# Performance work log

Measured on AMD Instinct MI355X. Metric: run time of the kernel, lower is better.

Reference implementation:

```python
import jax, jax.numpy as jnp
import numpy as np

B, S, D = 4, 4096, 64


def setup_inputs() -> dict:
    key = jax.random.key(0)
    ks = jax.random.split(key, 12)
    sc = 1.0 / np.sqrt(D)
    return {
        "q": jax.random.normal(ks[0], (B, S, D), jnp.float32),
        "k": jax.random.normal(ks[1], (B, S, D), jnp.float32),
        "v": jax.random.normal(ks[2], (B, S, D), jnp.float32),
        "attn_mask": jnp.ones((1, 1, 1), jnp.float32),
        "Wq": jax.random.normal(ks[3], (D, D), jnp.float32) * sc,
        "bq": jax.random.normal(ks[4], (D,), jnp.float32) * 0.01,
        "Wk": jax.random.normal(ks[5], (D, D), jnp.float32) * sc,
        "bk": jax.random.normal(ks[6], (D,), jnp.float32) * 0.01,
        "Wv": jax.random.normal(ks[7], (D, D), jnp.float32) * sc,
        "bv": jax.random.normal(ks[8], (D,), jnp.float32) * 0.01,
        "qw": jax.random.normal(ks[9], (1, 1, D), jnp.float32),
        "kw": jax.random.normal(ks[10], (1, 1, D), jnp.float32),
    }


def reference(q, k, v, attn_mask, Wq, bq, Wk, bk, Wv, bv, qw, kw):
    d = q.shape[-1]
    # Linear projections (torch Linear: x @ W.T + b)
    qp = q @ Wq.T + bq                      # (B,S,D)
    kp = k @ Wk.T + bk                      # (B,S,D)
    # learned per-feature elementwise weighting + 1/d scaling
    qwd = (qw * qp) / d                     # (B,S,D)
    kwd = (kw * kp) / d                     # (B,S,D)
    scores = jnp.einsum("bsd,btd->bst", qwd, kwd) + attn_mask  # (B,S,S)
    attn = jax.nn.softmax(scores, axis=-1)
    vp = v @ Wv.T + bv                      # (B,S,D)
    return jnp.einsum("bst,btd->bsd", attn, vp)
```

## Files before the change

kernel.cpp:

```cpp
#include <hip/hip_runtime.h>
#include <hip/hip_bf16.h>

typedef __attribute__((ext_vector_type(8)))  short    s16x8;
typedef __attribute__((ext_vector_type(4)))  short    s16x4;
typedef __attribute__((ext_vector_type(16))) float    f32x16;
typedef __attribute__((ext_vector_type(4)))  unsigned u32x4;
typedef __attribute__((ext_vector_type(2)))  unsigned u32x2;

#define NB 4
#define NS 4096
#define ND 64
#define NTOK (NB*NS)
#define PERB (NS*ND)

static __device__ __forceinline__ unsigned cvt_pk_bf16(float lo, float hi) {
    unsigned r;
    asm("v_cvt_pk_bf16_f32 %0, %1, %2" : "=v"(r) : "v"(lo), "v"(hi));
    return r;
}
static __device__ __forceinline__ float exp2_fast(float x) {
    float r;
    asm("v_exp_f32 %0, %1" : "=v"(r) : "v"(x));
    return r;
}

__global__ __launch_bounds__(64) void proj_kernel(
    const float* __restrict__ q, const float* __restrict__ k, const float* __restrict__ v,
    const float* __restrict__ Wq, const float* __restrict__ bq,
    const float* __restrict__ Wk, const float* __restrict__ bk,
    const float* __restrict__ Wv, const float* __restrict__ bv,
    const float* __restrict__ qw, const float* __restrict__ kw,
    __hip_bfloat16* __restrict__ qf, __hip_bfloat16* __restrict__ kf,
    __hip_bfloat16* __restrict__ vf)
{
    const int which = blockIdx.y;
    const int lane = threadIdx.x;
    const int r31 = lane & 31, hi = lane >> 5;
    const int bx = blockIdx.x;
    const float* X    = (which == 0) ? q  : (which == 1) ? k  : v;
    const float* W    = (which == 0) ? Wq : (which == 1) ? Wk : Wv;
    const float* bias = (which == 0) ? bq : (which == 1) ? bk : bv;

    const float* xrow = X + ((size_t)bx*32 + r31) * ND + 8*hi;
    s16x8 xf[4];
    #pragma unroll
    for (int c = 0; c < 4; ++c) {
        float4 f0 = *(const float4*)(xrow + 16*c);
        float4 f1 = *(const float4*)(xrow + 16*c + 4);
        u32x4 u = { cvt_pk_bf16(f0.x, f0.y), cvt_pk_bf16(f0.z, f0.w),
                    cvt_pk_bf16(f1.x, f1.y), cvt_pk_bf16(f1.z, f1.w) };
        xf[c] = __builtin_bit_cast(s16x8, u);
    }
    s16x8 wf[2][4];
    #pragma unroll
    for (int dt = 0; dt < 2; ++dt) {
        const float* wrow = W + (size_t)(32*dt + r31) * ND + 8*hi;
        #pragma unroll
        for (int c = 0; c < 4; ++c) {
            float4 f0 = *(const float4*)(wrow + 16*c);
            float4 f1 = *(const float4*)(wrow + 16*c + 4);
            u32x4 u = { cvt_pk_bf16(f0.x, f0.y), cvt_pk_bf16(f0.z, f0.w),
                        cvt_pk_bf16(f1.x, f1.y), cvt_pk_bf16(f1.z, f1.w) };
            wf[dt][c] = __builtin_bit_cast(s16x8, u);
        }
    }

    f32x16 acc0 = (f32x16)0.f, acc1 = (f32x16)0.f;

    if (which == 2) {
        #pragma unroll
        for (int c = 0; c < 4; ++c) {
            acc0 = __builtin_amdgcn_mfma_f32_32x32x16_bf16(xf[c], wf[0][c], acc0, 0, 0, 0);
            acc1 = __builtin_amdgcn_mfma_f32_32x32x16_bf16(xf[c], wf[1][c], acc1, 0, 0, 0);
        }
        const float b0 = bias[r31], b1 = bias[32 + r31];
        __hip_bfloat16* dst = vf + (size_t)(bx >> 1)*4096 + (bx & 1)*1024
                                 + r31*8 + 4*hi;
        #pragma unroll
        for (int g = 0; g < 4; ++g) {
            u32x2 p0 = { cvt_pk_bf16(acc0[4*g]   + b0, acc0[4*g+1] + b0),
                         cvt_pk_bf16(acc0[4*g+2] + b0, acc0[4*g+3] + b0) };
            *(s16x4*)(dst + (g >> 1)*512 + (g & 1)*256) = __builtin_bit_cast(s16x4, p0);
            u32x2 p1 = { cvt_pk_bf16(acc1[4*g]   + b1, acc1[4*g+1] + b1),
                         cvt_pk_bf16(acc1[4*g+2] + b1, acc1[4*g+3] + b1) };
            *(s16x4*)(dst + 2048 + (g >> 1)*512 + (g & 1)*256) = __builtin_bit_cast(s16x4, p1);
        }
    } else {
        #pragma unroll
        for (int c = 0; c < 4; ++c) {
            acc0 = __builtin_amdgcn_mfma_f32_32x32x16_bf16(wf[0][c], xf[c], acc0, 0, 0, 0);
            acc1 = __builtin_amdgcn_mfma_f32_32x32x16_bf16(wf[1][c], xf[c], acc1, 0, 0, 0);
        }
        const float* sc = (which == 0) ? qw : kw;
        const float cf = (which == 0) ? (0.015625f * 1.44269504088896f) : 0.015625f;
        __hip_bfloat16* dst = ((which == 0) ? qf : kf) + (size_t)bx*2048 + r31*8 + 4*hi;
        #pragma unroll
        for (int dt = 0; dt < 2; ++dt) {
            const f32x16 acc = dt ? acc1 : acc0;
            #pragma unroll
            for (int g = 0; g < 4; ++g) {
                const int dbase = 32*dt + 8*g + 4*hi;
                float4 b4 = *(const float4*)(bias + dbase);
                float4 s4 = *(const float4*)(sc + dbase);
                float v0 = (acc[4*g+0] + b4.x) * (s4.x * cf);
                float v1 = (acc[4*g+1] + b4.y) * (s4.y * cf);
                float v2 = (acc[4*g+2] + b4.z) * (s4.z * cf);
                float v3 = (acc[4*g+3] + b4.w) * (s4.w * cf);
                u32x2 p = { cvt_pk_bf16(v0, v1), cvt_pk_bf16(v2, v3) };
                *(s16x4*)(dst + (4*dt + g)*256) = __builtin_bit_cast(s16x4, p);
            }
        }
    }
}

__global__ __launch_bounds__(64, 4) void attn_kernel(
    const __hip_bfloat16* __restrict__ qf, const __hip_bfloat16* __restrict__ kf,
    const __hip_bfloat16* __restrict__ vf,
    float* __restrict__ opart, float* __restrict__ lpart,
    float* __restrict__ outdirect, int nsplit)
{
    const int lane = threadIdx.x;
    const int r31 = lane & 31, hi = lane >> 5;
    const int bid = blockIdx.x;
    const int b     = bid & 3;
    const int qwi   = (bid >> 2) & 127;
    const int split = bid >> 9;

    const __hip_bfloat16* qb = qf + (size_t)b*PERB;
    const __hip_bfloat16* kb = kf + (size_t)b*PERB;
    const __hip_bfloat16* vb = vf + (size_t)b*PERB;

    const __hip_bfloat16* qr = qb + (size_t)qwi*2048 + hi*256 + r31*8;
    s16x8 bQ[4];
    #pragma unroll
    for (int c = 0; c < 4; ++c) bQ[c] = *(const s16x8*)(qr + c*512);

    f32x16 O0 = (f32x16)0.f, O1 = (f32x16)0.f;
    float l = 0.f;

    const int span  = NS / nsplit;
    const int tbeg  = split * span;
    const int iters = span >> 6;

    for (int it = 0; it < iters; ++it) {
        const int tb = tbeg + (it << 6);

        const __hip_bfloat16* kbase = kb + (size_t)(tb >> 5)*2048 + hi*256 + r31*8;
        f32x16 s0 = (f32x16)0.f, s1 = (f32x16)0.f;
        #pragma unroll
        for (int c = 0; c < 4; ++c) {
            s16x8 a0 = *(const s16x8*)(kbase + c*512);
            s16x8 a1 = *(const s16x8*)(kbase + 2048 + c*512);
            s0 = __builtin_amdgcn_mfma_f32_32x32x16_bf16(a0, bQ[c], s0, 0, 0, 0);
            s1 = __builtin_amdgcn_mfma_f32_32x32x16_bf16(a1, bQ[c], s1, 0, 0, 0);
        }

        #pragma unroll
        for (int r = 0; r < 16; ++r) { s0[r] = exp2_fast(s0[r]); s1[r] = exp2_fast(s1[r]); }
        float t0 = ((s0[0]+s0[1])+(s0[2]+s0[3])) + ((s0[4]+s0[5])+(s0[6]+s0[7]));
        float t1 = ((s0[8]+s0[9])+(s0[10]+s0[11])) + ((s0[12]+s0[13])+(s0[14]+s0[15]));
        float t2 = ((s1[0]+s1[1])+(s1[2]+s1[3])) + ((s1[4]+s1[5])+(s1[6]+s1[7]));
        float t3 = ((s1[8]+s1[9])+(s1[10]+s1[11])) + ((s1[12]+s1[13])+(s1[14]+s1[15]));
        float rs = (t0 + t1) + (t2 + t3);
        rs += __shfl_xor(rs, 32);
        l += rs;

        unsigned pw0[2][4], pw1[2][4];
        #pragma unroll
        for (int u = 0; u < 4; ++u) {
            pw0[0][u] = cvt_pk_bf16(s0[4*u],   s0[4*u+1]);
            pw1[0][u] = cvt_pk_bf16(s0[4*u+2], s0[4*u+3]);
            pw0[1][u] = cvt_pk_bf16(s1[4*u],   s1[4*u+1]);
            pw1[1][u] = cvt_pk_bf16(s1[4*u+2], s1[4*u+3]);
        }

        const __hip_bfloat16* vbase = vb + (size_t)(tb >> 6)*4096 + hi*256 + r31*8;
        #pragma unroll
        for (int ks = 0; ks < 4; ++ks) {
            const int tl = ks >> 1, k1 = ks & 1;
            unsigned x0 = pw0[tl][2*k1], y0 = pw0[tl][2*k1 + 1];
            unsigned x1 = pw1[tl][2*k1], y1 = pw1[tl][2*k1 + 1];
            asm("v_permlane32_swap_b32 %0, %1" : "+v"(x0), "+v"(y0));
            asm("v_permlane32_swap_b32 %0, %1" : "+v"(x1), "+v"(y1));
            u32x4 fv = {x0, x1, y0, y1};
            s16x8 bP = __builtin_bit_cast(s16x8, fv);
            s16x8 a0 = *(const s16x8*)(vbase + ks*512);
            s16x8 a1 = *(const s16x8*)(vbase + 2048 + ks*512);
            O0 = __builtin_amdgcn_mfma_f32_32x32x16_bf16(a0, bP, O0, 0, 0, 0);
            O1 = __builtin_amdgcn_mfma_f32_32x32x16_bf16(a1, bP, O1, 0, 0, 0);
        }
    }

    const int qrow = qwi * 32 + r31;
    const size_t gq = (size_t)b*NS + qrow;
    if (outdirect) {
        const float invl = 1.f / l;
        float* orow = outdirect + gq * ND;
        #pragma unroll
        for (int u = 0; u < 4; ++u) {
            const int d0 = 8*u + 4*hi;
            float4 w0v = {O0[4*u]*invl, O0[4*u+1]*invl, O0[4*u+2]*invl, O0[4*u+3]*invl};
            *(float4*)(orow + d0) = w0v;
            float4 w1v = {O1[4*u]*invl, O1[4*u+1]*invl, O1[4*u+2]*invl, O1[4*u+3]*invl};
            *(float4*)(orow + d0 + 32) = w1v;
        }
    } else {
        float* prow = opart + ((size_t)split*NTOK + gq) * ND;
        #pragma unroll
        for (int u = 0; u < 4; ++u) {
            const int d0 = 8*u + 4*hi;
            float4 w0v = {O0[4*u], O0[4*u+1], O0[4*u+2], O0[4*u+3]};
            *(float4*)(prow + d0) = w0v;
            float4 w1v = {O1[4*u], O1[4*u+1], O1[4*u+2], O1[4*u+3]};
            *(float4*)(prow + d0 + 32) = w1v;
        }
        if (lane < 32) lpart[(size_t)split*NTOK + gq] = l;
    }
}

__global__ __launch_bounds__(256) void combine_kernel(
    const float* __restrict__ opart, const float* __restrict__ lpart,
    float* __restrict__ out, int nsplit)
{
    const int tid = threadIdx.x;
    const int r = blockIdx.x * 16 + (tid >> 4);
    const int c = (tid & 15) * 4;
    float L = 0.f;
    float4 acc = {0.f, 0.f, 0.f, 0.f};
    #pragma unroll
    for (int s = 0; s < 8; ++s) {
        if (s >= nsplit) break;
        L += lpart[(size_t)s*NTOK + r];
        float4 o = *(const float4*)(opart + ((size_t)s*NTOK + r)*ND + c);
        acc.x += o.x; acc.y += o.y; acc.z += o.z; acc.w += o.w;
    }
    const float inv = 1.f / L;
    float4 res = {acc.x*inv, acc.y*inv, acc.z*inv, acc.w*inv};
    *(float4*)(out + (size_t)r*ND + c) = res;
}

extern "C" void kernel_launch(void* const* d_in, const int* in_sizes, int n_in,
                              void* d_out, int out_size, void* d_ws, size_t ws_size,
                              hipStream_t stream) {
    (void)in_sizes; (void)n_in; (void)out_size;
    const float* q  = (const float*)d_in[0];
    const float* k  = (const float*)d_in[1];
    const float* v  = (const float*)d_in[2];
    const float* Wq = (const float*)d_in[4];
    const float* bq = (const float*)d_in[5];
    const float* Wk = (const float*)d_in[6];
    const float* bk = (const float*)d_in[7];
    const float* Wv = (const float*)d_in[8];
    const float* bv = (const float*)d_in[9];
    const float* qw = (const float*)d_in[10];
    const float* kw = (const float*)d_in[11];

    __hip_bfloat16* qfb = (__hip_bfloat16*)d_ws;
    __hip_bfloat16* kfb = qfb + (size_t)NTOK*ND;
    __hip_bfloat16* vfb = kfb + (size_t)NTOK*ND;
    float* rest = (float*)(vfb + (size_t)NTOK*ND);

    auto need = [](int s) {
        return (size_t)NTOK*ND*2*3 + (size_t)s*NTOK*(ND*4 + 4);
    };
    const int nsplit = (ws_size >= need(8)) ? 8
                     : (ws_size >= need(4)) ? 4
                     : (ws_size >= need(2)) ? 2 : 1;

    float* opart = rest;
    float* lp = opart + (size_t)nsplit*NTOK*ND;

    proj_kernel<<<dim3(512, 3), 64, 0, stream>>>(q, k, v, Wq, bq, Wk, bk, Wv, bv,
                                                 qw, kw, qfb, kfb, vfb);
    attn_kernel<<<dim3(512*nsplit), 64, 0, stream>>>(
        qfb, kfb, vfb, opart, lp,
        (nsplit == 1) ? (float*)d_out : nullptr, nsplit);
    if (nsplit > 1)
        combine_kernel<<<dim3(NTOK/16), 256, 0, stream>>>(opart, lp,
                                                          (float*)d_out, nsplit);
}
```

Before: 115.7 us.

## Share K/V tiles across 8 waves via LDS with direct global-to-LDS loads

After: 116.6 us. No clear change (+0.8%).

```diff
diff --git a/kernel.cpp b/kernel.cpp
--- a/kernel.cpp
+++ b/kernel.cpp
@@ -22,6 +22,12 @@
     float r;
     asm("v_exp_f32 %0, %1" : "=v"(r) : "v"(x));
     return r;
+}
+static __device__ __forceinline__ void gload_lds16(const __hip_bfloat16* g,
+                                                   __hip_bfloat16* l) {
+    __builtin_amdgcn_global_load_lds(
+        (const __attribute__((address_space(1))) unsigned int*)g,
+        (__attribute__((address_space(3))) unsigned int*)l, 16, 0, 0);
 }
 
 __global__ __launch_bounds__(64) void proj_kernel(
@@ -113,18 +119,24 @@
     }
 }
 
-__global__ __launch_bounds__(64, 4) void attn_kernel(
+__global__ __launch_bounds__(512, 4) void attn_kernel(
     const __hip_bfloat16* __restrict__ qf, const __hip_bfloat16* __restrict__ kf,
     const __hip_bfloat16* __restrict__ vf,
     float* __restrict__ opart, float* __restrict__ lpart,
     float* __restrict__ outdirect, int nsplit)
 {
-    const int lane = threadIdx.x;
+    __shared__ __hip_bfloat16 Klds[4096];
+    __shared__ __hip_bfloat16 Vlds[4096];
+
+    const int tid  = threadIdx.x;
+    const int lane = tid & 63;
+    const int wv   = tid >> 6;
     const int r31 = lane & 31, hi = lane >> 5;
     const int bid = blockIdx.x;
     const int b     = bid & 3;
-    const int qwi   = (bid >> 2) & 127;
-    const int split = bid >> 9;
+    const int qblk  = (bid >> 2) & 15;
+    const int split = bid >> 6;
+    const int qwi   = qblk * 8 + wv;
 
     const __hip_bfloat16* qb = qf + (size_t)b*PERB;
     const __hip_bfloat16* kb = kf + (size_t)b*PERB;
@@ -145,12 +157,17 @@
     for (int it = 0; it < iters; ++it) {
         const int tb = tbeg + (it << 6);
 
-        const __hip_bfloat16* kbase = kb + (size_t)(tb >> 5)*2048 + hi*256 + r31*8;
+        __syncthreads();
+        gload_lds16(kb + (size_t)(tb >> 5)*2048 + wv*512 + lane*8, &Klds[wv*512]);
+        gload_lds16(vb + (size_t)(tb >> 6)*4096 + wv*512 + lane*8, &Vlds[wv*512]);
+        __syncthreads();
+
+        const __hip_bfloat16* kl = Klds + hi*256 + r31*8;
         f32x16 s0 = (f32x16)0.f, s1 = (f32x16)0.f;
         #pragma unroll
         for (int c = 0; c < 4; ++c) {
-            s16x8 a0 = *(const s16x8*)(kbase + c*512);
-            s16x8 a1 = *(const s16x8*)(kbase + 2048 + c*512);
+            s16x8 a0 = *(const s16x8*)(kl + c*512);
+            s16x8 a1 = *(const s16x8*)(kl + 2048 + c*512);
             s0 = __builtin_amdgcn_mfma_f32_32x32x16_bf16(a0, bQ[c], s0, 0, 0, 0);
             s1 = __builtin_amdgcn_mfma_f32_32x32x16_bf16(a1, bQ[c], s1, 0, 0, 0);
         }
@@ -174,7 +191,7 @@
             pw1[1][u] = cvt_pk_bf16(s1[4*u+2], s1[4*u+3]);
         }
 
-        const __hip_bfloat16* vbase = vb + (size_t)(tb >> 6)*4096 + hi*256 + r31*8;
+        const __hip_bfloat16* vl = Vlds + hi*256 + r31*8;
         #pragma unroll
         for (int ks = 0; ks < 4; ++ks) {
             const int tl = ks >> 1, k1 = ks & 1;
@@ -184,8 +201,8 @@
             asm("v_permlane32_swap_b32 %0, %1" : "+v"(x1), "+v"(y1));
             u32x4 fv = {x0, x1, y0, y1};
             s16x8 bP = __builtin_bit_cast(s16x8, fv);
-            s16x8 a0 = *(const s16x8*)(vbase + ks*512);
-            s16x8 a1 = *(const s16x8*)(vbase + 2048 + ks*512);
+            s16x8 a0 = *(const s16x8*)(vl + ks*512);
+            s16x8 a1 = *(const s16x8*)(vl + 2048 + ks*512);
             O0 = __builtin_amdgcn_mfma_f32_32x32x16_bf16(a0, bP, O0, 0, 0, 0);
             O1 = __builtin_amdgcn_mfma_f32_32x32x16_bf16(a1, bP, O1, 0, 0, 0);
         }
@@ -272,7 +289,7 @@
 
     proj_kernel<<<dim3(512, 3), 64, 0, stream>>>(q, k, v, Wq, bq, Wk, bk, Wv, bv,
                                                  qw, kw, qfb, kfb, vfb);
-    attn_kernel<<<dim3(512*nsplit), 64, 0, stream>>>(
+    attn_kernel<<<dim3(64*nsplit), 512, 0, stream>>>(
         qfb, kfb, vfb, opart, lp,
         (nsplit == 1) ? (float*)d_out : nullptr, nsplit);
     if (nsplit > 1)
```
